# Performance work log

Measured on AMD Instinct MI355X. Metric: run time of the kernel, lower is better.

The kernel has to match this reference:

```python
import jax, jax.numpy as jnp
import numpy as np

DEPTH = 6
N_LEAVES = 2 ** DEPTH


def setup_inputs() -> dict:
    key = jax.random.key(0)
    ks = jax.random.split(key, 7)
    in_f, lw, out_f = 1024, 64, 512
    B = 4096
    s1 = 1.0 / np.sqrt(in_f)
    s2 = 1.0 / np.sqrt(lw)
    return {
        "x": jax.random.normal(ks[0], (B, in_f), jnp.float32),
        "node_weights": jax.random.uniform(ks[1], (N_LEAVES - 1, in_f), jnp.float32, -s1, s1),
        "node_biases": jax.random.uniform(ks[2], (N_LEAVES - 1, 1), jnp.float32, -s1, s1),
        "w1s": jax.random.uniform(ks[3], (N_LEAVES, in_f, lw), jnp.float32, -s1, s1),
        "b1s": jax.random.uniform(ks[4], (N_LEAVES, lw), jnp.float32, -s1, s1),
        "w2s": jax.random.uniform(ks[5], (N_LEAVES, lw, out_f), jnp.float32, -s2, s2),
        "b2s": jax.random.uniform(ks[6], (N_LEAVES, out_f), jnp.float32, -s2, s2),
    }


def _fff_forward(x, node_weights, node_biases, w1s, b1s, w2s, b2s):
    B = x.shape[0]
    # Soft routing: build per-leaf mixture weights level by level (training path).
    mixture = jnp.ones((B, N_LEAVES), x.dtype)
    for d in range(DEPTH):
        platform = 2 ** d - 1
        n_nodes = 2 ** d
        w = node_weights[platform:platform + n_nodes]          # (n, in)
        b = node_biases[platform:platform + n_nodes]            # (n, 1)
        logits = x @ w.T + b.T                                  # (B, n)
        be = jax.nn.sigmoid(logits)
        mod = jnp.stack([1.0 - be, be], axis=-1).reshape(B, 2 * n_nodes)
        mixture = (mixture.reshape(B, 2 * n_nodes, N_LEAVES // (2 * n_nodes))
                   * mod[:, :, None]).reshape(B, N_LEAVES)
    # All-leaf expert MLPs (grouped GEMMs), then mixture-weighted sum.
    h = jax.nn.relu(jnp.einsum('bi,liw->blw', x, w1s) + b1s[None])   # (B, L, W)
    y = jnp.einsum('blw,lwo->blo', h, w2s) + b2s[None]                # (B, L, O)
    return jnp.sum(y * mixture[:, :, None], axis=1)                   # (B, O)


def reference(x, node_weights, node_biases, w1s, b1s, w2s, b2s):
    return _fff_forward(x, node_weights, node_biases, w1s, b1s, w2s, b2s)
```

## Files before the change

### kernel.cpp

```cpp
#include <hip/hip_runtime.h>
#include <hip/hip_bf16.h>

typedef unsigned short u16;
typedef __attribute__((ext_vector_type(8))) short bf16x8;
typedef __attribute__((ext_vector_type(4))) float f32x4;
typedef __attribute__((ext_vector_type(16))) float f32x16;
typedef __attribute__((ext_vector_type(4))) unsigned short u16x4;
typedef __attribute__((ext_vector_type(8))) unsigned short u16x8;

#define BATCH 4096
#define INF   1024
#define NH    4096
#define OUTF  512
#define NLEAF 64
#define FDEPTH 6
#define ZSPL  4

__device__ __align__(16) u16  g_Xb[(size_t)BATCH * INF];
__device__ __align__(16) u16  g_W1t[(size_t)NH * INF];
__device__ __align__(16) u16  g_W2t[(size_t)OUTF * NH];
__device__ __align__(16) u16  g_NWh[(size_t)64 * INF];
__device__ __align__(16) u16  g_B2t[(size_t)OUTF * 64];
__device__ __align__(16) u16  g_Hb[(size_t)BATCH * NH];
__device__ __align__(16) float g_mix[(size_t)BATCH * NLEAF];
__device__ __align__(16) float g_part[(size_t)ZSPL * BATCH * OUTF];

__device__ inline u16 f2b(float f) {
  __hip_bfloat16 h = __float2bfloat16(f);
  return *reinterpret_cast<u16*>(&h);
}

__device__ inline void async16(const u16* g, u16* l) {
  __builtin_amdgcn_global_load_lds((const __attribute__((address_space(1))) void*)g,
                                   (__attribute__((address_space(3))) void*)l, 16, 0, 0);
}

__global__ __launch_bounds__(256) void prep_kernel(
    const float* __restrict__ x, const float* __restrict__ nw,
    const float* __restrict__ w1s, const float* __restrict__ w2s,
    const float* __restrict__ b2s) {
  __shared__ float tile[64 * 65];
  const int b = blockIdx.x;
  const int t = threadIdx.x;

  if (b < 2048) {
    int i = (b * 256 + t) * 8;
    float4 v0 = *(const float4*)(x + i);
    float4 v1 = *(const float4*)(x + i + 4);
    u16x8 h;
    h[0] = f2b(v0.x); h[1] = f2b(v0.y); h[2] = f2b(v0.z); h[3] = f2b(v0.w);
    h[4] = f2b(v1.x); h[5] = f2b(v1.y); h[6] = f2b(v1.z); h[7] = f2b(v1.w);
    *(u16x8*)(g_Xb + i) = h;
    return;
  }
  if (b < 2112) {
    int idx = ((b - 2048) * 256 + t) * 4;
    int n = idx >> 10;
    float4 v = make_float4(0.f, 0.f, 0.f, 0.f);
    if (n < 63) v = *(const float4*)(nw + idx);
    u16x4 h;
    h[0] = f2b(v.x); h[1] = f2b(v.y); h[2] = f2b(v.z); h[3] = f2b(v.w);
    *(u16x4*)(g_NWh + idx) = h;
    return;
  }

  const float* sb;
  u16* db;
  int R, C, r0, c0;
  if (b < 3136) {
    int idx = b - 2112;
    int z = idx >> 4;
    R = 1024; C = 64;
    r0 = (idx & 15) * 64; c0 = 0;
    sb = w1s + (size_t)z * R * C;
    db = g_W1t + (size_t)z * R * C;
  } else if (b < 3648) {
    int idx = b - 3136;
    R = 4096; C = 512;
    r0 = (idx >> 3) * 64; c0 = (idx & 7) * 64;
    sb = w2s;
    db = g_W2t;
  } else {
    int idx = b - 3648;
    R = 64; C = 512;
    r0 = 0; c0 = idx * 64;
    sb = b2s;
    db = g_B2t;
  }
  int cc4 = (t & 15) * 4;
#pragma unroll
  for (int it = 0; it < 4; ++it) {
    int rr = (t >> 4) + it * 16;
    float4 v = *(const float4*)(sb + (size_t)(r0 + rr) * C + c0 + cc4);
    tile[rr * 65 + cc4 + 0] = v.x;
    tile[rr * 65 + cc4 + 1] = v.y;
    tile[rr * 65 + cc4 + 2] = v.z;
    tile[rr * 65 + cc4 + 3] = v.w;
  }
  __syncthreads();
  int cc = t >> 2, rch = (t & 3) * 16;
  u16x8 o0, o1;
#pragma unroll
  for (int j = 0; j < 8; ++j) o0[j] = f2b(tile[(rch + j) * 65 + cc]);
#pragma unroll
  for (int j = 0; j < 8; ++j) o1[j] = f2b(tile[(rch + 8 + j) * 65 + cc]);
  u16* p = db + (size_t)(c0 + cc) * R + r0 + rch;
  *(u16x8*)p = o0;
  *(u16x8*)(p + 8) = o1;
}

__global__ __launch_bounds__(256) void mixture_kernel(
    const float* __restrict__ nb, float* __restrict__ out) {
  __shared__ __align__(16) unsigned char lds[57344];
  const int t = threadIdx.x;
  const int wv = t >> 6, ln = t & 63;
  const int quad = ln >> 4, m16 = ln & 15;
  const int r0 = blockIdx.x * 16;

  u16* stW = (u16*)(lds + wv * 10240);
  u16* stX = (u16*)(lds + wv * 10240 + 8192);
  float* lred = (float*)lds;
  float* ssig = (float*)(lds + 16384);
  u16* smixb = (u16*)(lds + 20480);
  u16* b2l = (u16*)(lds + 24576);

  f32x4 acc[4] = {};
#pragma unroll 1
  for (int it = 0; it < 4; ++it) {
    int kc = wv * 256 + it * 64;
#pragma unroll
    for (int j = 0; j < 8; ++j) {
      int id = j * 64 + ln;
      int row = id >> 3, c8 = (id & 7) ^ (row & 7);
      async16(g_NWh + (size_t)row * INF + kc + c8 * 8, stW + j * 512);
    }
#pragma unroll
    for (int j = 0; j < 2; ++j) {
      int id = j * 64 + ln;
      int row = id >> 3, c8 = (id & 7) ^ (row & 7);
      async16(g_Xb + (size_t)(r0 + row) * INF + kc + c8 * 8, stX + j * 512);
    }
    __syncthreads();
#pragma unroll
    for (int ks = 0; ks < 2; ++ks) {
      bf16x8 bF = *(const bf16x8*)(stX + m16 * 64 + ((ks * 4 + quad) ^ (m16 & 7)) * 8);
#pragma unroll
      for (int tw = 0; tw < 4; ++tw) {
        int row = tw * 16 + m16;
        bf16x8 aF = *(const bf16x8*)(stW + row * 64 + ((ks * 4 + quad) ^ (row & 7)) * 8);
        acc[tw] = __builtin_amdgcn_mfma_f32_16x16x32_bf16(aF, bF, acc[tw], 0, 0, 0);
      }
    }
    __syncthreads();
  }
#pragma unroll
  for (int tw = 0; tw < 4; ++tw)
#pragma unroll
    for (int r = 0; r < 4; ++r)
      lred[((size_t)wv * 64 + tw * 16 + quad * 4 + r) * 16 + m16] = acc[tw][r];
  __syncthreads();

#pragma unroll
  for (int j = 0; j < 8; ++j) {
    int id = (wv * 8 + j) * 64 + ln;
    int row = id >> 3, c8 = (id & 7) ^ (row & 7);
    async16(g_B2t + (size_t)row * 64 + c8 * 8, b2l + (wv * 8 + j) * 512);
  }

  {
    int n = t & 63, rg = t >> 6;
#pragma unroll
    for (int rr = 0; rr < 4; ++rr) {
      int row = rg * 4 + rr;
      float s = lred[(0 * 64 + n) * 16 + row] + lred[(1 * 64 + n) * 16 + row] +
                lred[(2 * 64 + n) * 16 + row] + lred[(3 * 64 + n) * 16 + row];
      if (n < 63) s += nb[n];
      ssig[row * 64 + n] = 1.f / (1.f + __expf(-s));
    }
  }
  __syncthreads();
  {
    int leaf = t & 63, rg = t >> 6;
#pragma unroll
    for (int rr = 0; rr < 4; ++rr) {
      int row = rg * 4 + rr;
      float p = 1.f;
#pragma unroll
      for (int d = 0; d < FDEPTH; ++d) {
        int node = (1 << d) - 1 + (leaf >> (FDEPTH - d));
        int bit = (leaf >> (FDEPTH - 1 - d)) & 1;
        float s = ssig[row * 64 + node];
        p *= bit ? s : (1.f - s);
      }
      g_mix[(size_t)(r0 + row) * 64 + leaf] = p;
      smixb[row * 64 + ((leaf >> 3) ^ (row & 7)) * 8 + (leaf & 7)] = f2b(p);
    }
  }
  __syncthreads();

  bf16x8 mixF[2];
#pragma unroll
  for (int ks = 0; ks < 2; ++ks)
    mixF[ks] = *(const bf16x8*)(smixb + m16 * 64 + ((ks * 4 + quad) ^ (m16 & 7)) * 8);
#pragma unroll 1
  for (int s = 0; s < 2; ++s) {
    f32x4 sacc[4] = {};
#pragma unroll
    for (int tile = 0; tile < 4; ++tile) {
#pragma unroll
      for (int ks = 0; ks < 2; ++ks) {
        int lrow = wv * 64 + tile * 16 + m16;
        bf16x8 aF = *(const bf16x8*)(b2l + lrow * 64 + ((ks * 4 + quad) ^ (lrow & 7)) * 8);
        sacc[tile] = __builtin_amdgcn_mfma_f32_16x16x32_bf16(aF, mixF[ks], sacc[tile], 0, 0, 0);
      }
    }
#pragma unroll
    for (int tile = 0; tile < 4; ++tile) {
      int o = s * 256 + wv * 64 + tile * 16 + quad * 4;
      *(f32x4*)(out + (size_t)(r0 + m16) * OUTF + o) = sacc[tile];
    }
    if (s == 0) {
      __syncthreads();
#pragma unroll
      for (int j = 0; j < 8; ++j) {
        int id = (wv * 8 + j) * 64 + ln;
        int row = id >> 3, c8 = (id & 7) ^ (row & 7);
        async16(g_B2t + (size_t)(256 + row) * 64 + c8 * 8, b2l + (wv * 8 + j) * 512);
      }
      __syncthreads();
    }
  }
}

__global__ __launch_bounds__(512, 2) void gemm1_kernel(const float* __restrict__ b1) {
  __shared__ __align__(16) u16 s_lds[65536];
  u16* lsA = s_lds;
  u16* lsB = s_lds + 32768;

  const int t = threadIdx.x;
  const int wv = t >> 6, ln = t & 63;
  const int quad = ln >> 4, m16 = ln & 15;
  const int wm = wv >> 2, wn = wv & 3;
  const int xcd = blockIdx.x & 7, slot = blockIdx.x >> 3;
  const int M0 = ((xcd >> 1) * 4 + (slot & 3)) * 256;
  const int N0 = ((xcd & 1) * 8 + (slot >> 2)) * 256;

  const int rhalf = ln >> 2;
  const int qg = (ln & 3) ^ ((ln >> 3) & 3);
  const u16* pA = g_W1t + (size_t)(M0 + wv * 32 + rhalf) * 1024 + qg * 8;
  const u16* pB = g_Xb + (size_t)(N0 + wv * 32 + rhalf) * 1024 + qg * 8;
  const int dst0 = wv * 1024;

  const int qx = (quad ^ ((m16 >> 1) & 3)) * 8;
  const int aro = (wm * 128 + m16) * 32 + qx;
  const int bro = (wn * 64 + m16) * 32 + qx;

  f32x4 acc[8][4] = {};
  bf16x8 bF[4];

#define STAGE_A(SLOT, TCOL)                                \
  do {                                                     \
    const u16* gs = pA + (TCOL);                           \
    u16* dd = lsA + (SLOT) * 8192 + dst0;                  \
    async16(gs, dd);                                       \
    async16(gs + 16 * 1024, dd + 512);                     \
  } while (0)
#define STAGE_B(SLOT, TCOL)                                \
  do {                                                     \
    const u16* gs = pB + (TCOL);                           \
    u16* dd = lsB + (SLOT) * 8192 + dst0;                  \
    async16(gs, dd);                                       \
    async16(gs + 16 * 1024, dd + 512);                     \
  } while (0)

#define G1_PHASE(ASLOT, BSLOT, AH, RELOAD_B, STAGE_STMT, VMCNT_STMT)        \
  {                                                                         \
    const u16* Abase = lsA + (ASLOT) * 8192;                                \
    bf16x8 aF[4];                                                           \
    _Pragma("unroll") for (int f = 0; f < 4; ++f)                           \
        aF[f] = *(const bf16x8*)(Abase + aro + ((AH) * 4 + f) * 512);       \
    if (RELOAD_B) {                                                         \
      const u16* Bbase = lsB + (BSLOT) * 8192;                              \
      _Pragma("unroll") for (int f = 0; f < 4; ++f)                         \
          bF[f] = *(const bf16x8*)(Bbase + bro + f * 512);                  \
    }                                                                       \
    STAGE_STMT;                                                             \
    __builtin_amdgcn_s_barrier();                                           \
    asm volatile("s_waitcnt lgkmcnt(0)" ::: "memory");                      \
    __builtin_amdgcn_s_setprio(1);                                          \
    _Pragma("unroll") for (int f = 0; f < 4; ++f)                           \
        _Pragma("unroll") for (int g = 0; g < 4; ++g)                       \
            acc[(AH) * 4 + f][g] = __builtin_amdgcn_mfma_f32_16x16x32_bf16( \
                aF[f], bF[g], acc[(AH) * 4 + f][g], 0, 0, 0);               \
    __builtin_amdgcn_s_setprio(0);                                          \
    VMCNT_STMT;                                                             \
    __builtin_amdgcn_s_barrier();                                           \
  }

  STAGE_B(0, 0);
  STAGE_A(0, 0);
  STAGE_B(1, 32);
  STAGE_A(1, 32);
  STAGE_B(2, 64);
  STAGE_A(2, 64);
  STAGE_B(3, 96);
  asm volatile("s_waitcnt vmcnt(6)" ::: "memory");
  __builtin_amdgcn_s_barrier();

#pragma unroll 1
  for (int i = 0; i < 8; ++i) {
    const int c1 = (2 * i + 1) * 64;
    const int c2 = ((2 * i + 2) & 15) * 64;
    const int c3 = ((2 * i + 3) & 15) * 64;
    G1_PHASE(0, 0, 0, 1, STAGE_A(3, c1 + 32), (void)0);
    G1_PHASE(0, 0, 1, 0, STAGE_B(0, c2), (void)0);
    G1_PHASE(1, 1, 0, 1, STAGE_A(0, c2), (void)0);
    G1_PHASE(1, 1, 1, 0, STAGE_B(1, c2 + 32),
             asm volatile("s_waitcnt vmcnt(6)" ::: "memory"));
    G1_PHASE(2, 2, 0, 1, STAGE_A(1, c2 + 32), (void)0);
    G1_PHASE(2, 2, 1, 0, STAGE_B(2, c3), (void)0);
    G1_PHASE(3, 3, 0, 1, STAGE_A(2, c3), (void)0);
    G1_PHASE(3, 3, 1, 0, STAGE_B(3, c3 + 32),
             asm volatile("s_waitcnt vmcnt(6)" ::: "memory"));
  }
#undef G1_PHASE
#undef STAGE_A
#undef STAGE_B

  asm volatile("s_waitcnt vmcnt(0)" ::: "memory");

  const int lb = (M0 >> 6) + wm * 2;
  float2 mx[4];
#pragma unroll
  for (int fb = 0; fb < 4; ++fb) {
    int bb = N0 + wn * 64 + fb * 16 + m16;
    mx[fb] = *(const float2*)(g_mix + (size_t)bb * 64 + lb);
  }
#pragma unroll
  for (int fa = 0; fa < 8; ++fa) {
    int n0 = M0 + wm * 128 + fa * 16 + quad * 4;
    float4 b1v = *(const float4*)(b1 + n0);
#pragma unroll
    for (int fb = 0; fb < 4; ++fb) {
      int bb = N0 + wn * 64 + fb * 16 + m16;
      float mixv = (fa < 4) ? mx[fb].x : mx[fb].y;
      u16x4 pk;
      pk[0] = f2b(fmaxf(acc[fa][fb][0] + b1v.x, 0.f) * mixv);
      pk[1] = f2b(fmaxf(acc[fa][fb][1] + b1v.y, 0.f) * mixv);
      pk[2] = f2b(fmaxf(acc[fa][fb][2] + b1v.z, 0.f) * mixv);
      pk[3] = f2b(fmaxf(acc[fa][fb][3] + b1v.w, 0.f) * mixv);
      *(u16x4*)(g_Hb + (size_t)bb * NH + n0) = pk;
    }
  }
}

__global__ __launch_bounds__(512, 2) void gemm2_kernel() {
  __shared__ __align__(16) u16 s_lds[49152];
  u16* lsA = s_lds;
  u16* lsB = s_lds + 32768;

  const int t = threadIdx.x;
  const int wv = t >> 6, ln = t & 63;
  const int quad = ln >> 4, m16 = ln & 15;
  const int wm = wv >> 2, wn = wv & 3;
  const int xcd = blockIdx.x & 7, slot = blockIdx.x >> 3;
  const int btile = xcd * 4 + (slot >> 3);
  const int rem = slot & 7;
  const int mtile = rem & 1, zidx = rem >> 1;
  const int N0 = btile * 128;
  const int M0 = mtile * 256;
  const int kbeg = zidx * 1024;

  const int rhalf = ln >> 2;
  const int qg = (ln & 3) ^ ((ln >> 3) & 3);
  const u16* pA = g_W2t + (size_t)(M0 + wv * 32 + rhalf) * 4096 + kbeg + qg * 8;
  const u16* pB = g_Hb + (size_t)(N0 + wv * 16 + rhalf) * 4096 + kbeg + qg * 8;
  const int dstA = wv * 1024;
  const int dstB = wv * 512;

  const int qx = (quad ^ ((m16 >> 1) & 3)) * 8;
  const int aro = (wm * 128 + m16) * 32 + qx;
  const int bro = (wn * 32 + m16) * 32 + qx;

  f32x4 acc[8][2] = {};
  bf16x8 bF[2];

#define STAGE_A2(SLOT, TCOL)                               \
  do {                                                     \
    const u16* gs = pA + (TCOL);                           \
    u16* dd = lsA + (SLOT) * 8192 + dstA;                  \
    async16(gs, dd);                                       \
    async16(gs + 16 * 4096, dd + 512);                     \
  } while (0)
#define STAGE_B2(SLOT, TCOL)                               \
  do {                                                     \
    const u16* gs = pB + (TCOL);                           \
    u16* dd = lsB + (SLOT) * 4096 + dstB;                  \
    async16(gs, dd);                                       \
  } while (0)

#define G2_PHASE(ASLOT, BSLOT, AH, RELOAD_B, STAGE_STMT, VMCNT_STMT)        \
  {                                                                         \
    const u16* Abase = lsA + (ASLOT) * 8192;                                \
    bf16x8 aF[4];                                                           \
    _Pragma("unroll") for (int f = 0; f < 4; ++f)                           \
        aF[f] = *(const bf16x8*)(Abase + aro + ((AH) * 4 + f) * 512);       \
    if (RELOAD_B) {                                                         \
      const u16* Bbase = lsB + (BSLOT) * 4096;                              \
      _Pragma("unroll") for (int g = 0; g < 2; ++g)                         \
          bF[g] = *(const bf16x8*)(Bbase + bro + g * 512);                  \
    }                                                                       \
    STAGE_STMT;                                                             \
    __builtin_amdgcn_s_barrier();                                           \
    asm volatile("s_waitcnt lgkmcnt(0)" ::: "memory");                      \
    __builtin_amdgcn_s_setprio(1);                                          \
    _Pragma("unroll") for (int f = 0; f < 4; ++f)                           \
        _Pragma("unroll") for (int g = 0; g < 2; ++g)                       \
            acc[(AH) * 4 + f][g] = __builtin_amdgcn_mfma_f32_16x16x32_bf16( \
                aF[f], bF[g], acc[(AH) * 4 + f][g], 0, 0, 0);               \
    __builtin_amdgcn_s_setprio(0);                                          \
    VMCNT_STMT;                                                             \
    __builtin_amdgcn_s_barrier();                                           \
  }

  STAGE_B2(0, 0);
  STAGE_A2(0, 0);
  STAGE_B2(1, 32);
  STAGE_A2(1, 32);
  STAGE_B2(2, 64);
  STAGE_A2(2, 64);
  STAGE_B2(3, 96);
  asm volatile("s_waitcnt vmcnt(4)" ::: "memory");
  __builtin_amdgcn_s_barrier();

#pragma unroll 1
  for (int i = 0; i < 8; ++i) {
    const int c1 = (2 * i + 1) * 64;
    const int c2 = ((2 * i + 2) & 15) * 64;
    const int c3 = ((2 * i + 3) & 15) * 64;
    G2_PHASE(0, 0, 0, 1, STAGE_A2(3, c1 + 32), (void)0);
    G2_PHASE(0, 0, 1, 0, STAGE_B2(0, c2), (void)0);
    G2_PHASE(1, 1, 0, 1, STAGE_A2(0, c2), (void)0);
    G2_PHASE(1, 1, 1, 0, STAGE_B2(1, c2 + 32),
             asm volatile("s_waitcnt vmcnt(4)" ::: "memory"));
    G2_PHASE(2, 2, 0, 1, STAGE_A2(1, c2 + 32), (void)0);
    G2_PHASE(2, 2, 1, 0, STAGE_B2(2, c3), (void)0);
    G2_PHASE(3, 3, 0, 1, STAGE_A2(2, c3), (void)0);
    G2_PHASE(3, 3, 1, 0, STAGE_B2(3, c3 + 32),
             asm volatile("s_waitcnt vmcnt(4)" ::: "memory"));
  }
#undef G2_PHASE
#undef STAGE_A2
#undef STAGE_B2

  asm volatile("s_waitcnt vmcnt(0)" ::: "memory");

  float* part = g_part + (size_t)zidx * ((size_t)BATCH * OUTF);
#pragma unroll
  for (int fa = 0; fa < 8; ++fa) {
    int og = M0 + wm * 128 + fa * 16 + quad * 4;
#pragma unroll
    for (int fb = 0; fb < 2; ++fb) {
      int bg = N0 + wn * 32 + fb * 16 + m16;
      *(f32x4*)(part + (size_t)bg * OUTF + og) = acc[fa][fb];
    }
  }
}

__global__ __launch_bounds__(256) void reduce_kernel(float* __restrict__ out) {
  int i = (blockIdx.x * 256 + threadIdx.x) * 4;
  float4 s = *(const float4*)(out + i);
#pragma unroll
  for (int z = 0; z < ZSPL; ++z) {
    const float4 p = *(const float4*)(g_part + (size_t)z * BATCH * OUTF + i);
    s.x += p.x; s.y += p.y; s.z += p.z; s.w += p.w;
  }
  *(float4*)(out + i) = s;
}

extern "C" void kernel_launch(void* const* d_in, const int* in_sizes, int n_in,
                              void* d_out, int out_size, void* d_ws, size_t ws_size,
                              hipStream_t stream) {
  const float* x = (const float*)d_in[0];
  const float* nw = (const float*)d_in[1];
  const float* nb = (const float*)d_in[2];
  const float* w1s = (const float*)d_in[3];
  const float* b1s = (const float*)d_in[4];
  const float* w2s = (const float*)d_in[5];
  const float* b2s = (const float*)d_in[6];
  float* out = (float*)d_out;
  (void)d_ws; (void)ws_size;

  hipLaunchKernelGGL(prep_kernel, dim3(3656), dim3(256), 0, stream,
                     x, nw, w1s, w2s, b2s);
  hipLaunchKernelGGL(mixture_kernel, dim3(256), dim3(256), 0, stream, nb, out);
  hipLaunchKernelGGL(gemm1_kernel, dim3(256), dim3(512), 0, stream, b1s);
  hipLaunchKernelGGL(gemm2_kernel, dim3(256), dim3(512), 0, stream);
  hipLaunchKernelGGL(reduce_kernel, dim3(2048), dim3(256), 0, stream, out);
}
```

Before: 188.5 us.

## Enlarge gemm2 batch tile to 256 and deepen split-K to eight

```diff
diff --git a/kernel.cpp b/kernel.cpp
--- a/kernel.cpp
+++ b/kernel.cpp
@@ -14,7 +14,7 @@
 #define OUTF  512
 #define NLEAF 64
 #define FDEPTH 6
-#define ZSPL  4
+#define ZSPL  8
 
 __device__ __align__(16) u16  g_Xb[(size_t)BATCH * INF];
 __device__ __align__(16) u16  g_W1t[(size_t)NH * INF];
@@ -44,13 +44,16 @@
   const int t = threadIdx.x;
 
   if (b < 2048) {
-    int i = (b * 256 + t) * 8;
-    float4 v0 = *(const float4*)(x + i);
-    float4 v1 = *(const float4*)(x + i + 4);
-    u16x8 h;
-    h[0] = f2b(v0.x); h[1] = f2b(v0.y); h[2] = f2b(v0.z); h[3] = f2b(v0.w);
-    h[4] = f2b(v1.x); h[5] = f2b(v1.y); h[6] = f2b(v1.z); h[7] = f2b(v1.w);
-    *(u16x8*)(g_Xb + i) = h;
+    int base = b * 2048;
+    int i0 = base + t * 4;
+    int i1 = base + 1024 + t * 4;
+    float4 v0 = *(const float4*)(x + i0);
+    float4 v1 = *(const float4*)(x + i1);
+    u16x4 h0, h1;
+    h0[0] = f2b(v0.x); h0[1] = f2b(v0.y); h0[2] = f2b(v0.z); h0[3] = f2b(v0.w);
+    h1[0] = f2b(v1.x); h1[1] = f2b(v1.y); h1[2] = f2b(v1.z); h1[3] = f2b(v1.w);
+    *(u16x4*)(g_Xb + i0) = h0;
+    *(u16x4*)(g_Xb + i1) = h1;
     return;
   }
   if (b < 2112) {
@@ -355,7 +358,7 @@
 }
 
 __global__ __launch_bounds__(512, 2) void gemm2_kernel() {
-  __shared__ __align__(16) u16 s_lds[49152];
+  __shared__ __align__(16) u16 s_lds[65536];
   u16* lsA = s_lds;
   u16* lsB = s_lds + 32768;
 
@@ -363,40 +366,37 @@
   const int wv = t >> 6, ln = t & 63;
   const int quad = ln >> 4, m16 = ln & 15;
   const int wm = wv >> 2, wn = wv & 3;
-  const int xcd = blockIdx.x & 7, slot = blockIdx.x >> 3;
-  const int btile = xcd * 4 + (slot >> 3);
-  const int rem = slot & 7;
-  const int mtile = rem & 1, zidx = rem >> 1;
-  const int N0 = btile * 128;
-  const int M0 = mtile * 256;
-  const int kbeg = zidx * 1024;
+  const int zidx = blockIdx.x & 7, slot = blockIdx.x >> 3;
+  const int M0 = (slot & 1) * 256;
+  const int N0 = (slot >> 1) * 256;
+  const int kbeg = zidx * 512;
 
   const int rhalf = ln >> 2;
   const int qg = (ln & 3) ^ ((ln >> 3) & 3);
   const u16* pA = g_W2t + (size_t)(M0 + wv * 32 + rhalf) * 4096 + kbeg + qg * 8;
-  const u16* pB = g_Hb + (size_t)(N0 + wv * 16 + rhalf) * 4096 + kbeg + qg * 8;
-  const int dstA = wv * 1024;
-  const int dstB = wv * 512;
+  const u16* pB = g_Hb + (size_t)(N0 + wv * 32 + rhalf) * 4096 + kbeg + qg * 8;
+  const int dst0 = wv * 1024;
 
   const int qx = (quad ^ ((m16 >> 1) & 3)) * 8;
   const int aro = (wm * 128 + m16) * 32 + qx;
-  const int bro = (wn * 32 + m16) * 32 + qx;
-
-  f32x4 acc[8][2] = {};
-  bf16x8 bF[2];
+  const int bro = (wn * 64 + m16) * 32 + qx;
+
+  f32x4 acc[8][4] = {};
+  bf16x8 bF[4];
 
 #define STAGE_A2(SLOT, TCOL)                               \
   do {                                                     \
     const u16* gs = pA + (TCOL);                           \
-    u16* dd = lsA + (SLOT) * 8192 + dstA;                  \
+    u16* dd = lsA + (SLOT) * 8192 + dst0;                  \
     async16(gs, dd);                                       \
     async16(gs + 16 * 4096, dd + 512);                     \
   } while (0)
 #define STAGE_B2(SLOT, TCOL)                               \
   do {                                                     \
     const u16* gs = pB + (TCOL);                           \
-    u16* dd = lsB + (SLOT) * 4096 + dstB;                  \
+    u16* dd = lsB + (SLOT) * 8192 + dst0;                  \
     async16(gs, dd);                                       \
+    async16(gs + 16 * 4096, dd + 512);                     \
   } while (0)
 
 #define G2_PHASE(ASLOT, BSLOT, AH, RELOAD_B, STAGE_STMT, VMCNT_STMT)        \
@@ -406,16 +406,16 @@
     _Pragma("unroll") for (int f = 0; f < 4; ++f)                           \
         aF[f] = *(const bf16x8*)(Abase + aro + ((AH) * 4 + f) * 512);       \
     if (RELOAD_B) {                                                         \
-      const u16* Bbase = lsB + (BSLOT) * 4096;                              \
-      _Pragma("unroll") for (int g = 0; g < 2; ++g)                         \
-          bF[g] = *(const bf16x8*)(Bbase + bro + g * 512);                  \
+      const u16* Bbase = lsB + (BSLOT) * 8192;                              \
+      _Pragma("unroll") for (int f = 0; f < 4; ++f)                         \
+          bF[f] = *(const bf16x8*)(Bbase + bro + f * 512);                  \
     }                                                                       \
     STAGE_STMT;                                                             \
     __builtin_amdgcn_s_barrier();                                           \
     asm volatile("s_waitcnt lgkmcnt(0)" ::: "memory");                      \
     __builtin_amdgcn_s_setprio(1);                                          \
     _Pragma("unroll") for (int f = 0; f < 4; ++f)                           \
-        _Pragma("unroll") for (int g = 0; g < 2; ++g)                       \
+        _Pragma("unroll") for (int g = 0; g < 4; ++g)                       \
             acc[(AH) * 4 + f][g] = __builtin_amdgcn_mfma_f32_16x16x32_bf16( \
                 aF[f], bF[g], acc[(AH) * 4 + f][g], 0, 0, 0);               \
     __builtin_amdgcn_s_setprio(0);                                          \
@@ -430,24 +430,24 @@
   STAGE_B2(2, 64);
   STAGE_A2(2, 64);
   STAGE_B2(3, 96);
-  asm volatile("s_waitcnt vmcnt(4)" ::: "memory");
+  asm volatile("s_waitcnt vmcnt(6)" ::: "memory");
   __builtin_amdgcn_s_barrier();
 
 #pragma unroll 1
-  for (int i = 0; i < 8; ++i) {
+  for (int i = 0; i < 4; ++i) {
     const int c1 = (2 * i + 1) * 64;
-    const int c2 = ((2 * i + 2) & 15) * 64;
-    const int c3 = ((2 * i + 3) & 15) * 64;
+    const int c2 = ((2 * i + 2) & 7) * 64;
+    const int c3 = ((2 * i + 3) & 7) * 64;
     G2_PHASE(0, 0, 0, 1, STAGE_A2(3, c1 + 32), (void)0);
     G2_PHASE(0, 0, 1, 0, STAGE_B2(0, c2), (void)0);
     G2_PHASE(1, 1, 0, 1, STAGE_A2(0, c2), (void)0);
     G2_PHASE(1, 1, 1, 0, STAGE_B2(1, c2 + 32),
-             asm volatile("s_waitcnt vmcnt(4)" ::: "memory"));
+             asm volatile("s_waitcnt vmcnt(6)" ::: "memory"));
     G2_PHASE(2, 2, 0, 1, STAGE_A2(1, c2 + 32), (void)0);
     G2_PHASE(2, 2, 1, 0, STAGE_B2(2, c3), (void)0);
     G2_PHASE(3, 3, 0, 1, STAGE_A2(2, c3), (void)0);
     G2_PHASE(3, 3, 1, 0, STAGE_B2(3, c3 + 32),
-             asm volatile("s_waitcnt vmcnt(4)" ::: "memory"));
+             asm volatile("s_waitcnt vmcnt(6)" ::: "memory"));
   }
 #undef G2_PHASE
 #undef STAGE_A2
@@ -460,8 +460,8 @@
   for (int fa = 0; fa < 8; ++fa) {
     int og = M0 + wm * 128 + fa * 16 + quad * 4;
 #pragma unroll
-    for (int fb = 0; fb < 2; ++fb) {
-      int bg = N0 + wn * 32 + fb * 16 + m16;
+    for (int fb = 0; fb < 4; ++fb) {
+      int bg = N0 + wn * 64 + fb * 16 + m16;
       *(f32x4*)(part + (size_t)bg * OUTF + og) = acc[fa][fb];
     }
   }
```

After: 205.0 us. 8.7% more time.

## Restructure GEMM1 main loop into four full-tile phases with 3-deep prefetch

Applied to the files above, without the earlier changes.

```diff
diff --git a/kernel.cpp b/kernel.cpp
--- a/kernel.cpp
+++ b/kernel.cpp
@@ -256,7 +256,6 @@
   const int bro = (wn * 64 + m16) * 32 + qx;
 
   f32x4 acc[8][4] = {};
-  bf16x8 bF[4];
 
 #define STAGE_A(SLOT, TCOL)                                \
   do {                                                     \
@@ -273,55 +272,46 @@
     async16(gs + 16 * 1024, dd + 512);                     \
   } while (0)
 
-#define G1_PHASE(ASLOT, BSLOT, AH, RELOAD_B, STAGE_STMT, VMCNT_STMT)        \
+#define G1_PHASE(SLOT, SC)                                                  \
   {                                                                         \
-    const u16* Abase = lsA + (ASLOT) * 8192;                                \
-    bf16x8 aF[4];                                                           \
-    _Pragma("unroll") for (int f = 0; f < 4; ++f)                           \
-        aF[f] = *(const bf16x8*)(Abase + aro + ((AH) * 4 + f) * 512);       \
-    if (RELOAD_B) {                                                         \
-      const u16* Bbase = lsB + (BSLOT) * 8192;                              \
-      _Pragma("unroll") for (int f = 0; f < 4; ++f)                         \
-          bF[f] = *(const bf16x8*)(Bbase + bro + f * 512);                  \
-    }                                                                       \
-    STAGE_STMT;                                                             \
+    const u16* Abase = lsA + (SLOT) * 8192;                                 \
+    const u16* Bbase = lsB + (SLOT) * 8192;                                 \
+    bf16x8 aF[8];                                                           \
+    _Pragma("unroll") for (int f = 0; f < 8; ++f)                           \
+        aF[f] = *(const bf16x8*)(Abase + aro + f * 512);                    \
+    bf16x8 bF[4];                                                           \
+    _Pragma("unroll") for (int g = 0; g < 4; ++g)                           \
+        bF[g] = *(const bf16x8*)(Bbase + bro + g * 512);                    \
+    STAGE_A((SC) & 3, ((SC) & 31) * 32);                                    \
+    STAGE_B((SC) & 3, ((SC) & 31) * 32);                                    \
     __builtin_amdgcn_s_barrier();                                           \
     asm volatile("s_waitcnt lgkmcnt(0)" ::: "memory");                      \
     __builtin_amdgcn_s_setprio(1);                                          \
-    _Pragma("unroll") for (int f = 0; f < 4; ++f)                           \
+    _Pragma("unroll") for (int f = 0; f < 8; ++f)                           \
         _Pragma("unroll") for (int g = 0; g < 4; ++g)                       \
-            acc[(AH) * 4 + f][g] = __builtin_amdgcn_mfma_f32_16x16x32_bf16( \
-                aF[f], bF[g], acc[(AH) * 4 + f][g], 0, 0, 0);               \
+            acc[f][g] = __builtin_amdgcn_mfma_f32_16x16x32_bf16(            \
+                aF[f], bF[g], acc[f][g], 0, 0, 0);                          \
     __builtin_amdgcn_s_setprio(0);                                          \
-    VMCNT_STMT;                                                             \
+    asm volatile("s_waitcnt vmcnt(8)" ::: "memory");                        \
     __builtin_amdgcn_s_barrier();                                           \
   }
 
+  STAGE_A(0, 0);
   STAGE_B(0, 0);
-  STAGE_A(0, 0);
+  STAGE_A(1, 32);
   STAGE_B(1, 32);
-  STAGE_A(1, 32);
+  STAGE_A(2, 64);
   STAGE_B(2, 64);
-  STAGE_A(2, 64);
-  STAGE_B(3, 96);
-  asm volatile("s_waitcnt vmcnt(6)" ::: "memory");
+  asm volatile("s_waitcnt vmcnt(8)" ::: "memory");
   __builtin_amdgcn_s_barrier();
 
 #pragma unroll 1
   for (int i = 0; i < 8; ++i) {
-    const int c1 = (2 * i + 1) * 64;
-    const int c2 = ((2 * i + 2) & 15) * 64;
-    const int c3 = ((2 * i + 3) & 15) * 64;
-    G1_PHASE(0, 0, 0, 1, STAGE_A(3, c1 + 32), (void)0);
-    G1_PHASE(0, 0, 1, 0, STAGE_B(0, c2), (void)0);
-    G1_PHASE(1, 1, 0, 1, STAGE_A(0, c2), (void)0);
-    G1_PHASE(1, 1, 1, 0, STAGE_B(1, c2 + 32),
-             asm volatile("s_waitcnt vmcnt(6)" ::: "memory"));
-    G1_PHASE(2, 2, 0, 1, STAGE_A(1, c2 + 32), (void)0);
-    G1_PHASE(2, 2, 1, 0, STAGE_B(2, c3), (void)0);
-    G1_PHASE(3, 3, 0, 1, STAGE_A(2, c3), (void)0);
-    G1_PHASE(3, 3, 1, 0, STAGE_B(3, c3 + 32),
-             asm volatile("s_waitcnt vmcnt(6)" ::: "memory"));
+    const int c = i * 4;
+    G1_PHASE(0, c + 3);
+    G1_PHASE(1, c + 4);
+    G1_PHASE(2, c + 5);
+    G1_PHASE(3, c + 6);
   }
 #undef G1_PHASE
 #undef STAGE_A
```

Measured after the change: 192.2 us. About the same (+2.0%).
